# Performance work log

Hardware: AMD Instinct MI355X
Metric: run time of the kernel (lower is better)

Reference implementation:

```python
import jax, jax.numpy as jnp
import numpy as np

NEG_SLOPE = 0.2  # PyG GATConv default


def _gat_layer(x, src, dst, W, a_s, a_d, b, num_nodes):
    H, C = a_s.shape
    h = (x @ W).reshape(num_nodes, H, C)                     # [N,H,C]
    alpha_src = jnp.einsum('nhc,hc->nh', h, a_s)             # [N,H]
    alpha_dst = jnp.einsum('nhc,hc->nh', h, a_d)             # [N,H]
    e = jax.nn.leaky_relu(alpha_src[src] + alpha_dst[dst], NEG_SLOPE)  # [E,H]
    # segment softmax over incoming edges of each destination node
    m = jax.lax.stop_gradient(jax.ops.segment_max(e, dst, num_segments=num_nodes))
    e = jnp.exp(e - m[dst])
    den = jax.ops.segment_sum(e, dst, num_segments=num_nodes)
    alpha = e / den[dst]                                     # [E,H]
    msg = h[src] * alpha[:, :, None]                         # [E,H,C]
    out = jax.ops.segment_sum(msg, dst, num_segments=num_nodes)
    return out.reshape(num_nodes, H * C) + b


def setup_inputs() -> dict:
    key = jax.random.key(0)
    ks = jax.random.split(key, 10)
    N, E, D, H, C = 100000, 1600000, 128, 4, 32
    s = 1.0 / np.sqrt(D)
    return {
        'x': jax.random.normal(ks[0], (N, D), jnp.float32),
        'edge_index': jax.random.randint(ks[1], (2, E), 0, N, jnp.int64),
        'W1': jax.random.normal(ks[2], (D, H * C), jnp.float32) * s,
        'a_src1': jax.random.normal(ks[3], (H, C), jnp.float32) * s,
        'a_dst1': jax.random.normal(ks[4], (H, C), jnp.float32) * s,
        'b1': jnp.zeros((H * C,), jnp.float32),
        'W2': jax.random.normal(ks[5], (H * C, H * C), jnp.float32) * s,
        'a_src2': jax.random.normal(ks[6], (H, C), jnp.float32) * s,
        'a_dst2': jax.random.normal(ks[7], (H, C), jnp.float32) * s,
        'b2': jnp.zeros((H * C,), jnp.float32),
    }


def reference(x, edge_index, W1, a_src1, a_dst1, b1, W2, a_src2, a_dst2, b2):
    N = x.shape[0]
    loop = jnp.arange(N, dtype=edge_index.dtype)  # PyG add_self_loops=True
    src = jnp.concatenate([edge_index[0], loop])
    dst = jnp.concatenate([edge_index[1], loop])
    h = _gat_layer(x, src, dst, W1, a_src1, a_dst1, b1, N)
    h = jax.nn.relu(h)
    h = _gat_layer(h, src, dst, W2, a_src2, a_dst2, b2, N)
    return jax.nn.relu(h)
```

## Files before the change

### kernel.cpp

```cpp
#include <hip/hip_runtime.h>
#include <cstdint>
#include <cstddef>

#define NEG_SLOPE 0.2f
#define BIN_SHIFT 9
#define BCAP 16384
#define LOG2E 1.4426950408889634f

typedef short bf16x8 __attribute__((ext_vector_type(8)));
typedef float f32x4 __attribute__((ext_vector_type(4)));

#if __has_builtin(__builtin_amdgcn_exp2f)
#define EXP2(x) __builtin_amdgcn_exp2f(x)
#else
#define EXP2(x) exp2f(x)
#endif

static __device__ __forceinline__ unsigned short bf16r(float f) {
    unsigned u = __float_as_uint(f);
    return (unsigned short)((u + 0x7fffu + ((u >> 16) & 1u)) >> 16);
}
static __device__ __forceinline__ float bfu_lo(unsigned u) { return __uint_as_float(u << 16); }
static __device__ __forceinline__ float bfu_hi(unsigned u) { return __uint_as_float(u & 0xffff0000u); }

__global__ __launch_bounds__(256) void wprep_k(const float* __restrict__ W1, const float* __restrict__ W2,
                                               unsigned short* __restrict__ Wh1, unsigned short* __restrict__ Wl1,
                                               unsigned short* __restrict__ Wh2, unsigned short* __restrict__ Wl2,
                                               int* __restrict__ bcnt) {
    if (blockIdx.x == 0) bcnt[threadIdx.x] = 0;
    int t = blockIdx.x * 256 + threadIdx.x;
    const float* W;
    unsigned short *Wh, *Wl;
    int idx;
    if (t < 16384) { W = W1; Wh = Wh1; Wl = Wl1; idx = t; }
    else           { W = W2; Wh = Wh2; Wl = Wl2; idx = t - 16384; }
    int c = idx >> 7;
    int k = idx & 127;
    float w = W[(size_t)k * 128 + c];
    unsigned short h = bf16r(w);
    float lo = w - __uint_as_float((unsigned)h << 16);
    int dst = (k >> 5) * 4096 + (c >> 4) * 512 + (((k >> 3) & 3) * 16 + (c & 15)) * 8 + (k & 7);
    Wh[dst] = h;
    Wl[dst] = bf16r(lo);
}

__global__ __launch_bounds__(256) void bin_k(const int* __restrict__ srcI, const int* __restrict__ dstI,
                                             int E, int N, int K, int* __restrict__ bcnt,
                                             int* __restrict__ tmpE) {
    __shared__ int hist[256];
    __shared__ int lbase[256];
    const int t = threadIdx.x;
    const int M = E + N;
    const int chunk0 = blockIdx.x * 4096;
    hist[t] = 0;
    __syncthreads();

    int s[16], d[16], b[16];
#pragma unroll
    for (int j = 0; j < 16; ++j) {
        int i = chunk0 + t + j * 256;
        b[j] = -1;
        if (i < M) {
            int ss, dd;
            if (i < E) { ss = srcI[i]; dd = dstI[i]; }
            else       { ss = i - E;  dd = ss; }
            if ((unsigned)dd < (unsigned)N && (unsigned)ss < (unsigned)N) {
                s[j] = ss; d[j] = dd; b[j] = dd >> BIN_SHIFT;
                atomicAdd(&hist[b[j]], 1);
            }
        }
    }
    __syncthreads();
    if (t < K) {
        int c = hist[t];
        lbase[t] = (c > 0) ? atomicAdd(&bcnt[t], c) : 0;
    }
    hist[t] = 0;
    __syncthreads();
#pragma unroll
    for (int j = 0; j < 16; ++j) {
        if (b[j] >= 0) {
            int r = atomicAdd(&hist[b[j]], 1);
            int pos = lbase[b[j]] + r;
            if (pos < BCAP) tmpE[(size_t)b[j] * BCAP + pos] = (s[j] << 9) | (d[j] & 511);
        }
    }
}

__global__ __launch_bounds__(256) void scatter_csr_k(const int* __restrict__ tmpE,
                                                     const int* __restrict__ bcnt,
                                                     int* __restrict__ rowptr,
                                                     int* __restrict__ colOff,
                                                     int N, int K) {
    __shared__ int pre[256];
    __shared__ int cur[512];
    __shared__ int ss[256];
    const int t = threadIdx.x;
    const int b = blockIdx.x;

    int bc = (t < K) ? min(bcnt[t], BCAP) : 0;
    pre[t] = bc;
    __syncthreads();
    for (int off = 1; off < 256; off <<= 1) {
        int v = (t >= off) ? pre[t - off] : 0;
        __syncthreads();
        pre[t] += v;
        __syncthreads();
    }
    const int base_b = (b == 0) ? 0 : pre[b - 1];
    const int cnt_b  = pre[b] - base_b;
    if (b == K - 1 && t == 0) rowptr[N] = pre[K - 1];

    const int nlo = b << BIN_SHIFT;
    const int nhi = min(nlo + (1 << BIN_SHIFT), N);
    const int nn  = nhi - nlo;
    const int* te = tmpE + (size_t)b * BCAP;

    cur[t] = 0;
    cur[t + 256] = 0;
    __syncthreads();
    for (int i = t; i < cnt_b; i += 256) atomicAdd(&cur[te[i] & 511], 1);
    __syncthreads();

    int v0 = cur[2 * t], v1 = cur[2 * t + 1];
    ss[t] = v0 + v1;
    __syncthreads();
    for (int off = 1; off < 256; off <<= 1) {
        int v = (t >= off) ? ss[t - off] : 0;
        __syncthreads();
        ss[t] += v;
        __syncthreads();
    }
    int e0 = (t == 0) ? 0 : ss[t - 1];
    int e1 = e0 + v0;
    if (2 * t < nn)     rowptr[nlo + 2 * t]     = base_b + e0;
    if (2 * t + 1 < nn) rowptr[nlo + 2 * t + 1] = base_b + e1;
    cur[2 * t] = e0;
    cur[2 * t + 1] = e1;
    __syncthreads();

    for (int i = t; i < cnt_b; i += 256) {
        int v = te[i];
        int r = atomicAdd(&cur[v & 511], 1);
        colOff[base_b + r] = ((unsigned)v >> 9) << 8;
    }
}

__global__ __launch_bounds__(256) void gemm_mfma_k(const float* __restrict__ X,
                                                   const unsigned short* __restrict__ Wh,
                                                   const unsigned short* __restrict__ Wl,
                                                   const float* __restrict__ a_s,
                                                   const float* __restrict__ a_d,
                                                   unsigned short* __restrict__ Hout,
                                                   float* __restrict__ asrc,
                                                   float* __restrict__ adst,
                                                   int N) {
    __shared__ __align__(16) unsigned short hstage[4][32][132];
    const int tid = threadIdx.x;
    const int wid = tid >> 6;
    const int l   = tid & 63;
    const int l15 = l & 15;
    const int lh  = l >> 4;
    const int waveRow = blockIdx.x * 128 + wid * 32;
    if (waveRow >= N) return;

    f32x4 acc[2][8];
#pragma unroll
    for (int m = 0; m < 2; ++m)
#pragma unroll
        for (int f = 0; f < 8; ++f)
#pragma unroll
            for (int c = 0; c < 4; ++c) acc[m][f][c] = 0.f;

    const int r0 = waveRow + l15;
    const int r1 = waveRow + 16 + l15;
    const size_t xoff0 = (size_t)min(r0, N - 1) * 128;
    const size_t xoff1 = (size_t)min(r1, N - 1) * 128;
    const int kb = lh * 8;

#pragma unroll
    for (int ks = 0; ks < 4; ++ks) {
        bf16x8 ah[2], al[2];
#pragma unroll
        for (int m = 0; m < 2; ++m) {
            const float* xp = X + (m ? xoff1 : xoff0) + ks * 32 + kb;
            float4 v0 = *(const float4*)xp;
            float4 v1 = *(const float4*)(xp + 4);
            float xs[8] = {v0.x, v0.y, v0.z, v0.w, v1.x, v1.y, v1.z, v1.w};
#pragma unroll
            for (int j = 0; j < 8; ++j) {
                unsigned short h = bf16r(xs[j]);
                float hf = __uint_as_float((unsigned)h << 16);
                ah[m][j] = (short)h;
                al[m][j] = (short)bf16r(xs[j] - hf);
            }
        }
        const unsigned short* wbh = Wh + ks * 4096 + l * 8;
        const unsigned short* wbl = Wl + ks * 4096 + l * 8;
#pragma unroll
        for (int f = 0; f < 8; ++f) {
            bf16x8 wh = *(const bf16x8*)(wbh + f * 512);
            bf16x8 wl = *(const bf16x8*)(wbl + f * 512);
#pragma unroll
            for (int m = 0; m < 2; ++m) {
                acc[m][f] = __builtin_amdgcn_mfma_f32_16x16x32_bf16(ah[m], wh, acc[m][f], 0, 0, 0);
                acc[m][f] = __builtin_amdgcn_mfma_f32_16x16x32_bf16(al[m], wh, acc[m][f], 0, 0, 0);
                acc[m][f] = __builtin_amdgcn_mfma_f32_16x16x32_bf16(ah[m], wl, acc[m][f], 0, 0, 0);
            }
        }
    }

    float asf[8], adf[8];
#pragma unroll
    for (int f = 0; f < 8; ++f) {
        asf[f] = a_s[f * 16 + l15];
        adf[f] = a_d[f * 16 + l15];
    }
    const int q = l15;
#pragma unroll
    for (int m = 0; m < 2; ++m) {
#pragma unroll
        for (int r = 0; r < 4; ++r) {
            float ps[4] = {0.f, 0.f, 0.f, 0.f};
            float pd[4] = {0.f, 0.f, 0.f, 0.f};
#pragma unroll
            for (int f = 0; f < 8; ++f) {
                float v = acc[m][f][r];
                ps[f >> 1] = fmaf(v, asf[f], ps[f >> 1]);
                pd[f >> 1] = fmaf(v, adf[f], pd[f >> 1]);
                hstage[wid][m * 16 + lh * 4 + r][f * 16 + l15] = bf16r(v);
            }
#pragma unroll
            for (int mask = 1; mask < 16; mask <<= 1) {
#pragma unroll
                for (int h = 0; h < 4; ++h) {
                    ps[h] += __shfl_xor(ps[h], mask);
                    pd[h] += __shfl_xor(pd[h], mask);
                }
            }
            int row = waveRow + m * 16 + lh * 4 + r;
            if (q < 8 && row < N) {
                float v0 = (q & 1) ? ps[1] : ps[0];
                float v1 = (q & 1) ? ps[3] : ps[2];
                float vs = (q & 2) ? v1 : v0;
                float w0 = (q & 1) ? pd[1] : pd[0];
                float w1 = (q & 1) ? pd[3] : pd[2];
                float vd = (q & 2) ? w1 : w0;
                if (q < 4) asrc[row * 4 + q] = vs * LOG2E;
                else       adst[row * 4 + (q - 4)] = vd * LOG2E;
            }
        }
    }

#pragma unroll
    for (int it = 0; it < 8; ++it) {
        int row = it * 4 + lh;
        const unsigned short* hp = &hstage[wid][row][l15 * 8];
        uint2 aa = *(const uint2*)hp;
        uint2 bb = *(const uint2*)(hp + 4);
        int grow = waveRow + row;
        if (grow < N) {
            uint4 o;
            o.x = aa.x; o.y = aa.y; o.z = bb.x; o.w = bb.y;
            *(uint4*)&Hout[(size_t)grow * 128 + l15 * 8] = o;
        }
    }
}

__global__ __launch_bounds__(256) void aggregate_k(const unsigned short* __restrict__ Hbuf,
                                                   const float* __restrict__ asrc,
                                                   const float* __restrict__ adst,
                                                   const int* __restrict__ rowptr,
                                                   const int* __restrict__ colOff,
                                                   const float* __restrict__ bias,
                                                   float* __restrict__ out, int N) {
    int wave = (blockIdx.x * 256 + threadIdx.x) >> 6;
    int lane = threadIdx.x & 63;
    if (wave >= N) return;
    const int n = wave;
    const int c0 = lane * 2;
    const int head = c0 >> 5;
    const float adh = adst[n * 4 + head];
    const char* Hb = (const char*)Hbuf;
    const char* As = (const char*)asrc;
    const int hoff = c0 * 2;
    const int aoff = head * 4;

    int b = __builtin_amdgcn_readfirstlane(rowptr[n]);
    int e = __builtin_amdgcn_readfirstlane(rowptr[n + 1]);
    float acc0 = 0.f, acc1 = 0.f, sw = 0.f;
    for (int p = b; p < e; p += 8) {
        int off[8];
#pragma unroll
        for (int j = 0; j < 8; ++j) off[j] = colOff[min(p + j, e - 1)];
        float a[8];
#pragma unroll
        for (int j = 0; j < 8; ++j) a[j] = *(const float*)(As + (off[j] >> 4) + aoff);
        unsigned hu[8];
#pragma unroll
        for (int j = 0; j < 8; ++j) hu[j] = *(const unsigned*)(Hb + off[j] + hoff);
#pragma unroll
        for (int j = 0; j < 8; ++j) {
            float x = a[j] + adh;
            float w = (p + j < e) ? EXP2(fmaxf(x, NEG_SLOPE * x)) : 0.f;
            sw += w;
            acc0 = fmaf(w, bfu_lo(hu[j]), acc0);
            acc1 = fmaf(w, bfu_hi(hu[j]), acc1);
        }
    }
    float inv = 1.f / sw;
    float o0 = fmaxf(acc0 * inv + bias[c0], 0.f);
    float o1 = fmaxf(acc1 * inv + bias[c0 + 1], 0.f);
    *(float2*)&out[(size_t)n * 128 + c0] = make_float2(o0, o1);
}


extern "C" void kernel_launch(void* const* d_in, const int* in_sizes, int n_in,
                              void* d_out, int out_size, void* d_ws, size_t ws_size,
                              hipStream_t stream) {
    const float* X   = (const float*)d_in[0];
    const int*   EI  = (const int*)d_in[1];
    const float* W1  = (const float*)d_in[2];
    const float* as1 = (const float*)d_in[3];
    const float* ad1 = (const float*)d_in[4];
    const float* b1  = (const float*)d_in[5];
    const float* W2  = (const float*)d_in[6];
    const float* as2 = (const float*)d_in[7];
    const float* ad2 = (const float*)d_in[8];
    const float* b2  = (const float*)d_in[9];

    const int N = in_sizes[0] / 128;
    const int E = in_sizes[1] / 2;
    const int M = E + N;
    const int K = (N + (1 << BIN_SHIFT) - 1) >> BIN_SHIFT;
    const int* srcI = EI;
    const int* dstI = EI + E;

    char* w = (char*)d_ws;
    auto alloc = [&](size_t bytes) {
        char* p = w;
        w += (bytes + 255) & ~(size_t)255;
        return p;
    };
    unsigned short* Hbuf = (unsigned short*)alloc((size_t)N * 128 * 2);
    float* asrc   = (float*)alloc((size_t)N * 4 * 4);
    float* adst   = (float*)alloc((size_t)N * 4 * 4);
    int*   rowptr = (int*)alloc((size_t)(N + 1) * 4);
    int*   colOff = (int*)alloc((size_t)M * 4);
    int*   tmpE   = (int*)alloc((size_t)K * BCAP * 4);
    int*   bcnt   = (int*)alloc(256 * 4);
    unsigned short* Wt1h = (unsigned short*)alloc(128 * 128 * 2);
    unsigned short* Wt1l = (unsigned short*)alloc(128 * 128 * 2);
    unsigned short* Wt2h = (unsigned short*)alloc(128 * 128 * 2);
    unsigned short* Wt2l = (unsigned short*)alloc(128 * 128 * 2);

    const int gemmBlocks = (N + 127) / 128;
    float* out = (float*)d_out;

    wprep_k<<<128, 256, 0, stream>>>(W1, W2, Wt1h, Wt1l, Wt2h, Wt2l, bcnt);
    bin_k<<<(M + 4095) / 4096, 256, 0, stream>>>(srcI, dstI, E, N, K, bcnt, tmpE);
    scatter_csr_k<<<K, 256, 0, stream>>>(tmpE, bcnt, rowptr, colOff, N, K);
    gemm_mfma_k<<<gemmBlocks, 256, 0, stream>>>(X, Wt1h, Wt1l, as1, ad1, Hbuf, asrc, adst, N);
    aggregate_k<<<((size_t)N * 64 + 255) / 256, 256, 0, stream>>>(Hbuf, asrc, adst, rowptr, colOff, b1, out, N);
    gemm_mfma_k<<<gemmBlocks, 256, 0, stream>>>(out, Wt2h, Wt2l, as2, ad2, Hbuf, asrc, adst, N);
    aggregate_k<<<((size_t)N * 64 + 255) / 256, 256, 0, stream>>>(Hbuf, asrc, adst, rowptr, colOff, b2, out, N);
}
```

Before: 378.6 us.

## Split bf16 features into per-head planes and aggregate per head

The GEMM now writes the bf16 projected features as four per-head planes of 64 bytes per node instead of one interleaved 256-byte row, and the CSR column offsets are rescaled to match. The aggregation kernel is restructured so each block handles one head for 16 nodes. Each wave processes 4 nodes, with 16-lane groups gathering different edges in parallel, followed by cross-group shuffle reductions. The aim is to make the gathered working set per head smaller and more cache-friendly and to fill gather bandwidth better. The cost is four passes over rowptr, colOff and the attention logits, plus extra shuffle work.

```diff
diff --git a/kernel.cpp b/kernel.cpp
--- a/kernel.cpp
+++ b/kernel.cpp
@@ -142,7 +142,7 @@
     for (int i = t; i < cnt_b; i += 256) {
         int v = te[i];
         int r = atomicAdd(&cur[v & 511], 1);
-        colOff[base_b + r] = ((unsigned)v >> 9) << 8;
+        colOff[base_b + r] = ((unsigned)v >> 9) << 6;
     }
 }
 
@@ -151,10 +151,10 @@
                                                    const unsigned short* __restrict__ Wl,
                                                    const float* __restrict__ a_s,
                                                    const float* __restrict__ a_d,
-                                                   unsigned short* __restrict__ Hout,
+                                                   char* __restrict__ Hout,
                                                    float* __restrict__ asrc,
                                                    float* __restrict__ adst,
-                                                   int N) {
+                                                   int N, int planeB) {
     __shared__ __align__(16) unsigned short hstage[4][32][132];
     const int tid = threadIdx.x;
     const int wid = tid >> 6;
@@ -262,56 +262,68 @@
         if (grow < N) {
             uint4 o;
             o.x = aa.x; o.y = aa.y; o.z = bb.x; o.w = bb.y;
-            *(uint4*)&Hout[(size_t)grow * 128 + l15 * 8] = o;
-        }
-    }
-}
-
-__global__ __launch_bounds__(256) void aggregate_k(const unsigned short* __restrict__ Hbuf,
+            char* dst = Hout + (size_t)(l15 >> 2) * planeB + (size_t)grow * 64 + (l15 & 3) * 16;
+            *(uint4*)dst = o;
+        }
+    }
+}
+
+__global__ __launch_bounds__(256) void aggregate_k(const char* __restrict__ Hb,
                                                    const float* __restrict__ asrc,
                                                    const float* __restrict__ adst,
                                                    const int* __restrict__ rowptr,
                                                    const int* __restrict__ colOff,
                                                    const float* __restrict__ bias,
-                                                   float* __restrict__ out, int N) {
-    int wave = (blockIdx.x * 256 + threadIdx.x) >> 6;
-    int lane = threadIdx.x & 63;
-    if (wave >= N) return;
-    const int n = wave;
-    const int c0 = lane * 2;
-    const int head = c0 >> 5;
-    const float adh = adst[n * 4 + head];
-    const char* Hb = (const char*)Hbuf;
+                                                   float* __restrict__ out, int N, int planeB) {
+    const int head = blockIdx.x & 3;
+    const int grp  = blockIdx.x >> 2;
+    const int wid  = threadIdx.x >> 6;
+    const int lane = threadIdx.x & 63;
+    const int g    = lane >> 4;
+    const int li   = lane & 15;
+    const char* plane = Hb + (size_t)head * planeB;
     const char* As = (const char*)asrc;
-    const int hoff = c0 * 2;
     const int aoff = head * 4;
-
-    int b = __builtin_amdgcn_readfirstlane(rowptr[n]);
-    int e = __builtin_amdgcn_readfirstlane(rowptr[n + 1]);
-    float acc0 = 0.f, acc1 = 0.f, sw = 0.f;
-    for (int p = b; p < e; p += 8) {
-        int off[8];
-#pragma unroll
-        for (int j = 0; j < 8; ++j) off[j] = colOff[min(p + j, e - 1)];
-        float a[8];
-#pragma unroll
-        for (int j = 0; j < 8; ++j) a[j] = *(const float*)(As + (off[j] >> 4) + aoff);
-        unsigned hu[8];
-#pragma unroll
-        for (int j = 0; j < 8; ++j) hu[j] = *(const unsigned*)(Hb + off[j] + hoff);
-#pragma unroll
-        for (int j = 0; j < 8; ++j) {
-            float x = a[j] + adh;
-            float w = (p + j < e) ? EXP2(fmaxf(x, NEG_SLOPE * x)) : 0.f;
-            sw += w;
-            acc0 = fmaf(w, bfu_lo(hu[j]), acc0);
-            acc1 = fmaf(w, bfu_hi(hu[j]), acc1);
-        }
-    }
-    float inv = 1.f / sw;
-    float o0 = fmaxf(acc0 * inv + bias[c0], 0.f);
-    float o1 = fmaxf(acc1 * inv + bias[c0 + 1], 0.f);
-    *(float2*)&out[(size_t)n * 128 + c0] = make_float2(o0, o1);
+    const int hoff = li * 4;
+    const float2 bv = *(const float2*)&bias[head * 32 + li * 2];
+
+    const int n0 = grp * 16 + wid * 4;
+#pragma unroll 1
+    for (int i = 0; i < 4; ++i) {
+        int n = n0 + i;
+        if (n >= N) break;
+        int b = __builtin_amdgcn_readfirstlane(rowptr[n]);
+        int e = __builtin_amdgcn_readfirstlane(rowptr[n + 1]);
+        float adh = adst[n * 4 + head];
+        float acc0 = 0.f, acc1 = 0.f, sw = 0.f;
+        for (int p = b; p < e; p += 8) {
+            int q0 = p + g, q1 = p + 4 + g;
+            int off0 = colOff[min(q0, e - 1)];
+            int off1 = colOff[min(q1, e - 1)];
+            float a0 = *(const float*)(As + (off0 >> 2) + aoff);
+            float a1 = *(const float*)(As + (off1 >> 2) + aoff);
+            unsigned u0 = *(const unsigned*)(plane + off0 + hoff);
+            unsigned u1 = *(const unsigned*)(plane + off1 + hoff);
+            float x0 = a0 + adh, x1 = a1 + adh;
+            float w0 = (q0 < e) ? EXP2(fmaxf(x0, NEG_SLOPE * x0)) : 0.f;
+            float w1 = (q1 < e) ? EXP2(fmaxf(x1, NEG_SLOPE * x1)) : 0.f;
+            sw += w0 + w1;
+            acc0 = fmaf(w0, bfu_lo(u0), acc0);
+            acc1 = fmaf(w0, bfu_hi(u0), acc1);
+            acc0 = fmaf(w1, bfu_lo(u1), acc0);
+            acc1 = fmaf(w1, bfu_hi(u1), acc1);
+        }
+        sw   += __shfl_xor(sw, 16);   sw   += __shfl_xor(sw, 32);
+        acc0 += __shfl_xor(acc0, 16); acc0 += __shfl_xor(acc0, 32);
+        acc1 += __shfl_xor(acc1, 16); acc1 += __shfl_xor(acc1, 32);
+        if (g == 0) {
+            float inv = 1.f / sw;
+            float2 o;
+            o.x = fmaxf(acc0 * inv + bv.x, 0.f);
+            o.y = fmaxf(acc1 * inv + bv.y, 0.f);
+            *(float2*)&out[(size_t)n * 128 + head * 32 + li * 2] = o;
+        }
+    }
 }
 
 
@@ -335,6 +347,7 @@
     const int K = (N + (1 << BIN_SHIFT) - 1) >> BIN_SHIFT;
     const int* srcI = EI;
     const int* dstI = EI + E;
+    const int planeB = N * 64;
 
     char* w = (char*)d_ws;
     auto alloc = [&](size_t bytes) {
@@ -342,7 +355,7 @@
         w += (bytes + 255) & ~(size_t)255;
         return p;
     };
-    unsigned short* Hbuf = (unsigned short*)alloc((size_t)N * 128 * 2);
+    char*  Hbuf   = (char*)alloc((size_t)N * 256);
     float* asrc   = (float*)alloc((size_t)N * 4 * 4);
     float* adst   = (float*)alloc((size_t)N * 4 * 4);
     int*   rowptr = (int*)alloc((size_t)(N + 1) * 4);
@@ -355,13 +368,14 @@
     unsigned short* Wt2l = (unsigned short*)alloc(128 * 128 * 2);
 
     const int gemmBlocks = (N + 127) / 128;
+    const int aggBlocks  = ((N + 15) / 16) * 4;
     float* out = (float*)d_out;
 
     wprep_k<<<128, 256, 0, stream>>>(W1, W2, Wt1h, Wt1l, Wt2h, Wt2l, bcnt);
     bin_k<<<(M + 4095) / 4096, 256, 0, stream>>>(srcI, dstI, E, N, K, bcnt, tmpE);
     scatter_csr_k<<<K, 256, 0, stream>>>(tmpE, bcnt, rowptr, colOff, N, K);
-    gemm_mfma_k<<<gemmBlocks, 256, 0, stream>>>(X, Wt1h, Wt1l, as1, ad1, Hbuf, asrc, adst, N);
-    aggregate_k<<<((size_t)N * 64 + 255) / 256, 256, 0, stream>>>(Hbuf, asrc, adst, rowptr, colOff, b1, out, N);
-    gemm_mfma_k<<<gemmBlocks, 256, 0, stream>>>(out, Wt2h, Wt2l, as2, ad2, Hbuf, asrc, adst, N);
-    aggregate_k<<<((size_t)N * 64 + 255) / 256, 256, 0, stream>>>(Hbuf, asrc, adst, rowptr, colOff, b2, out, N);
-}
+    gemm_mfma_k<<<gemmBlocks, 256, 0, stream>>>(X, Wt1h, Wt1l, as1, ad1, Hbuf, asrc, adst, N, planeB);
+    aggregate_k<<<aggBlocks, 256, 0, stream>>>(Hbuf, asrc, adst, rowptr, colOff, b1, out, N, planeB);
+    gemm_mfma_k<<<gemmBlocks, 256, 0, stream>>>(out, Wt2h, Wt2l, as2, ad2, Hbuf, asrc, adst, N, planeB);
+    aggregate_k<<<aggBlocks, 256, 0, stream>>>(Hbuf, asrc, adst, rowptr, colOff, b2, out, N, planeB);
+}
```

Measured after the change: 523.6 us. 1.38x slower.
